# Optimization experiments

Hardware: AMD Instinct MI355X
Metric: run time of the kernel (lower is better)

The kernel has to match this reference:

```python
import jax, jax.numpy as jnp
import numpy as np

HIDDEN = 256
HEADS = 8
HEAD_DIM = HIDDEN // HEADS


def setup_inputs() -> dict:
    key = jax.random.key(0)
    ks = jax.random.split(key, 8)
    B, N, L, C = 8, 512, 24, HIDDEN
    s = 1.0 / np.sqrt(C)
    return {
        "spatial_nodes": jax.random.normal(ks[0], (B, N, C), jnp.float32),
        "temporal_nodes": jax.random.normal(ks[1], (B, N, L, C), jnp.float32),
        "Wq": jax.random.normal(ks[2], (C, C), jnp.float32) * s,
        "bq": jnp.zeros((C,), jnp.float32),
        "Wkv": jax.random.normal(ks[3], (C, 2 * C), jnp.float32) * s,
        "bkv": jnp.zeros((2 * C,), jnp.float32),
        "Wo": jax.random.normal(ks[4], (C, C), jnp.float32) * s,
        "bo": jnp.zeros((C,), jnp.float32),
    }


def reference(spatial_nodes, temporal_nodes, Wq, bq, Wkv, bkv, Wo, bo):
    B, N, C = spatial_nodes.shape
    L = temporal_nodes.shape[2]
    H, D = HEADS, HEAD_DIM
    q = spatial_nodes @ Wq + bq                      # [B,N,C]
    kv = temporal_nodes @ Wkv + bkv                  # [B,N,L,2C]
    k, v = jnp.split(kv, 2, axis=-1)                 # each [B,N,L,C]
    q = q.reshape(B, N, H, D)
    k = k.reshape(B, N, L, H, D)
    v = v.reshape(B, N, L, H, D)
    scores = jnp.einsum('bnhd,bnlhd->bnhl', q, k) / jnp.sqrt(jnp.float32(D))
    attn = jax.nn.softmax(scores, axis=-1)           # dropout is identity in eval
    out = jnp.einsum('bnhl,bnlhd->bnhd', attn, v).reshape(B, N, C)
    return out @ Wo + bo
```

## Files before the change

### kernel.cpp

```cpp
#include <hip/hip_runtime.h>
#include <hip/hip_bf16.h>


#define L_ 24
#define C_ 256
#define H_ 8
#define D_ 32
#define NTOK 4096
#define SCALE 0.17677669529663687f

typedef __attribute__((ext_vector_type(8))) short short8;
typedef __attribute__((ext_vector_type(4))) float f32x4;

#define QK_OFF   ((size_t)0)
#define TBAR_OFF ((size_t)16777216)
#define MT_OFF   ((size_t)33554432)
#define W2T_OFF  ((size_t)34603008)
#define BQK_OFF  ((size_t)35651584)
#define BO2_OFF  ((size_t)35659776)
#define WS_NEED  ((size_t)35660800)

__global__ __launch_bounds__(256)
void k_pre(const float* __restrict__ Wq, const float* __restrict__ bq,
           const float* __restrict__ Wkv, const float* __restrict__ bkv,
           const float* __restrict__ Wo, const float* __restrict__ bo,
           char* __restrict__ ws)
{
    __hip_bfloat16* mt  = (__hip_bfloat16*)(ws + MT_OFF);
    __hip_bfloat16* w2t = (__hip_bfloat16*)(ws + W2T_OFF);
    float* bqk = (float*)(ws + BQK_OFF);
    float* bo2 = (float*)(ws + BO2_OFF);
    const int b = blockIdx.x, tid = threadIdx.x;
    __shared__ float sW[32][33];
    if (b < 128) {
        const bool isV = b >= 64;
        const int bb = isV ? b - 64 : b;
        const int h = bb >> 3, c0 = (bb & 7) * 32;
        {
            const int ci = tid >> 3, dq = (tid & 7) * 4;
            const float4 v = *(const float4*)(Wkv + (size_t)(c0 + ci) * 512 + (isV ? 256 : 0) + h * 32 + dq);
            sW[ci][dq + 0] = v.x; sW[ci][dq + 1] = v.y; sW[ci][dq + 2] = v.z; sW[ci][dq + 3] = v.w;
        }
        __syncthreads();
        const int e = tid;
        float wreg[32];
        if (!isV) {
#pragma unroll
            for (int dq = 0; dq < 32; dq += 4) {
                const float4 v = *(const float4*)(Wq + (size_t)e * 256 + h * 32 + dq);
                wreg[dq] = v.x; wreg[dq + 1] = v.y; wreg[dq + 2] = v.z; wreg[dq + 3] = v.w;
            }
            for (int ci = 0; ci < 32; ++ci) {
                float a = 0.f;
#pragma unroll
                for (int d = 0; d < 32; ++d) a = fmaf(wreg[d], sW[ci][d], a);
                mt[(size_t)(h * 256 + c0 + ci) * 256 + e] = __float2bfloat16(a * SCALE);
            }
        } else {
#pragma unroll
            for (int d = 0; d < 32; ++d) wreg[d] = Wo[(size_t)(h * 32 + d) * 256 + e];
            __hip_bfloat16 accs[32];
            for (int ci = 0; ci < 32; ++ci) {
                float a = 0.f;
#pragma unroll
                for (int d = 0; d < 32; ++d) a = fmaf(wreg[d], sW[ci][d], a);
                accs[ci] = __float2bfloat16(a);
            }
#pragma unroll
            for (int g = 0; g < 4; ++g)
                *(uint4*)&w2t[(size_t)e * 2048 + h * 256 + c0 + g * 8] = *(const uint4*)&accs[g * 8];
        }
    } else if (b == 128) {
        for (int o = 0; o < 8; ++o) {
            const int hc = o * 256 + tid;
            const int h = hc >> 8, c = hc & 255;
            float a = 0.f;
            for (int d = 0; d < 32; ++d)
                a = fmaf(bq[h * 32 + d], Wkv[(size_t)c * 512 + h * 32 + d], a);
            bqk[hc] = a * SCALE;
        }
    } else {
        const int e = tid;
        float a = bo[e];
        for (int hd = 0; hd < 256; ++hd)
            a = fmaf(bkv[256 + hd], Wo[(size_t)hd * 256 + e], a);
        bo2[e] = a;
    }
}

__global__ __launch_bounds__(256)
void k_qk(const float* __restrict__ S, char* __restrict__ ws)
{
    const __hip_bfloat16* mt = (const __hip_bfloat16*)(ws + MT_OFF);
    const float* bqk = (const float*)(ws + BQK_OFF);
    __hip_bfloat16* qk = (__hip_bfloat16*)(ws + QK_OFF);
    __shared__ __hip_bfloat16 sA[64][40];
    __shared__ __hip_bfloat16 sB[64][40];
    const int tid = threadIdx.x;
    const int bm = blockIdx.x & 63, bn = blockIdx.x >> 6;
    const int m0 = bm * 64, n0 = bn * 64;
    const int w = tid >> 6, L = tid & 63;
    const int wr = (w >> 1) * 32, wc = (w & 1) * 32;
    const int fr = L & 15, fk = (L >> 4) * 8;
    const int sr = tid >> 2, sc = (tid & 3) * 8;
    f32x4 acc[2][2] = {};
    for (int k0 = 0; k0 < 256; k0 += 32) {
        {
            const float* p = S + (size_t)(m0 + sr) * 256 + k0 + sc;
            const float4 v0 = *(const float4*)p, v1 = *(const float4*)(p + 4);
            union { __hip_bfloat16 h[8]; uint4 u; } pk;
            pk.h[0] = __float2bfloat16(v0.x); pk.h[1] = __float2bfloat16(v0.y);
            pk.h[2] = __float2bfloat16(v0.z); pk.h[3] = __float2bfloat16(v0.w);
            pk.h[4] = __float2bfloat16(v1.x); pk.h[5] = __float2bfloat16(v1.y);
            pk.h[6] = __float2bfloat16(v1.z); pk.h[7] = __float2bfloat16(v1.w);
            *(uint4*)&sA[sr][sc] = pk.u;
            *(uint4*)&sB[sr][sc] = *(const uint4*)(mt + (size_t)(n0 + sr) * 256 + k0 + sc);
        }
        __syncthreads();
        short8 af0 = *(const short8*)&sA[wr +  0 + fr][fk];
        short8 af1 = *(const short8*)&sA[wr + 16 + fr][fk];
        short8 bf0 = *(const short8*)&sB[wc +  0 + fr][fk];
        short8 bf1 = *(const short8*)&sB[wc + 16 + fr][fk];
        acc[0][0] = __builtin_amdgcn_mfma_f32_16x16x32_bf16(af0, bf0, acc[0][0], 0, 0, 0);
        acc[0][1] = __builtin_amdgcn_mfma_f32_16x16x32_bf16(af0, bf1, acc[0][1], 0, 0, 0);
        acc[1][0] = __builtin_amdgcn_mfma_f32_16x16x32_bf16(af1, bf0, acc[1][0], 0, 0, 0);
        acc[1][1] = __builtin_amdgcn_mfma_f32_16x16x32_bf16(af1, bf1, acc[1][1], 0, 0, 0);
        __syncthreads();
    }
#pragma unroll
    for (int i = 0; i < 2; ++i)
#pragma unroll
    for (int j = 0; j < 2; ++j) {
        const int col = n0 + wc + j * 16 + fr;
        const float bb = bqk[col];
#pragma unroll
        for (int r = 0; r < 4; ++r) {
            const int row = m0 + wr + i * 16 + (L >> 4) * 4 + r;
            qk[(size_t)row * 2048 + col] = __float2bfloat16(acc[i][j][r] + bb);
        }
    }
}

__global__ __launch_bounds__(256)
void k_attn(const float* __restrict__ T, char* __restrict__ ws)
{
    const __hip_bfloat16* qk = (const __hip_bfloat16*)(ws + QK_OFF);
    __hip_bfloat16* tbar = (__hip_bfloat16*)(ws + TBAR_OFF);
    __shared__ float            sT[24][260];
    __shared__ __hip_bfloat16   sTb[32][264];
    __shared__ __hip_bfloat16   sqk[16][264];
    __shared__ float            sAt[8][33];
    const int tid = threadIdx.x;
    const int t = blockIdx.x;
    {
        const float4* Tv = (const float4*)(T + (size_t)t * 6144);
#pragma unroll
        for (int k = 0; k < 6; ++k) {
            const int f = tid + k * 256;
            const float4 v = Tv[f];
            const int l = f >> 6, c = (f & 63) * 4;
            *(float4*)&sT[l][c] = v;
            __hip_bfloat16 b4[4] = { __float2bfloat16(v.x), __float2bfloat16(v.y),
                                     __float2bfloat16(v.z), __float2bfloat16(v.w) };
            *(uint2*)&sTb[l][c] = *(const uint2*)b4;
        }
    }
    {
        const int h = tid >> 5, c = (tid & 31) * 8;
        *(uint4*)&sqk[h][c] = *(const uint4*)(qk + (size_t)t * 2048 + tid * 8);
    }
    {
        const uint4 z = {0u, 0u, 0u, 0u};
        char* zq = (char*)&sqk[8][0];
        char* zt = (char*)&sTb[24][0];
        *(uint4*)(zq + tid * 16) = z;
        *(uint4*)(zt + tid * 16) = z;
        if (tid < 8) {
            *(uint4*)(zq + 4096 + tid * 16) = z;
            *(uint4*)(zt + 4096 + tid * 16) = z;
        }
    }
    __syncthreads();
    if (tid < 64) {
        const int fr = tid & 15, fk = (tid >> 4) * 8;
        f32x4 acc[2] = {};
#pragma unroll
        for (int ks = 0; ks < 8; ++ks) {
            const short8 a  = *(const short8*)&sqk[fr][ks * 32 + fk];
            const short8 b0 = *(const short8*)&sTb[fr][ks * 32 + fk];
            const short8 b1 = *(const short8*)&sTb[16 + fr][ks * 32 + fk];
            acc[0] = __builtin_amdgcn_mfma_f32_16x16x32_bf16(a, b0, acc[0], 0, 0, 0);
            acc[1] = __builtin_amdgcn_mfma_f32_16x16x32_bf16(a, b1, acc[1], 0, 0, 0);
        }
        if (tid < 32) {
            const int hb = (tid >> 4) * 4, l0 = tid & 15;
#pragma unroll
            for (int r = 0; r < 4; ++r) {
                sAt[hb + r][l0] = acc[0][r];
                if (l0 < 8) sAt[hb + r][16 + l0] = acc[1][r];
            }
        }
    }
    __syncthreads();
    if (tid < 8) {
        float mx = -1e30f;
#pragma unroll
        for (int l = 0; l < 24; ++l) mx = fmaxf(mx, sAt[tid][l]);
        float e[24]; float sum = 0.f;
#pragma unroll
        for (int l = 0; l < 24; ++l) { e[l] = __expf(sAt[tid][l] - mx); sum += e[l]; }
        const float inv = 1.0f / sum;
#pragma unroll
        for (int l = 0; l < 24; ++l) sAt[tid][l] = e[l] * inv;
    }
    __syncthreads();
    {
        const int h = tid >> 5, c0 = (tid & 31) * 8;
        float acc[8] = {};
        for (int l = 0; l < 24; ++l) {
            const float a = sAt[h][l];
            const float4 u = *(const float4*)&sT[l][c0];
            const float4 v = *(const float4*)&sT[l][c0 + 4];
            acc[0] = fmaf(a, u.x, acc[0]); acc[1] = fmaf(a, u.y, acc[1]);
            acc[2] = fmaf(a, u.z, acc[2]); acc[3] = fmaf(a, u.w, acc[3]);
            acc[4] = fmaf(a, v.x, acc[4]); acc[5] = fmaf(a, v.y, acc[5]);
            acc[6] = fmaf(a, v.z, acc[6]); acc[7] = fmaf(a, v.w, acc[7]);
        }
        union { __hip_bfloat16 h8[8]; uint4 u; } pk;
#pragma unroll
        for (int j = 0; j < 8; ++j) pk.h8[j] = __float2bfloat16(acc[j]);
        *(uint4*)&tbar[(size_t)t * 2048 + tid * 8] = pk.u;
    }
}

__global__ __launch_bounds__(256)
void k_out(const char* __restrict__ ws, float* __restrict__ Out)
{
    const __hip_bfloat16* tbar = (const __hip_bfloat16*)(ws + TBAR_OFF);
    const __hip_bfloat16* w2t  = (const __hip_bfloat16*)(ws + W2T_OFF);
    const float* bo2 = (const float*)(ws + BO2_OFF);
    __shared__ __hip_bfloat16 sA[64][72];
    __shared__ __hip_bfloat16 sB[32][72];
    const int tid = threadIdx.x;
    const int bm = blockIdx.x & 63, bn = blockIdx.x >> 6;
    const int m0 = bm * 64, n0 = bn * 32;
    const int w = tid >> 6, L = tid & 63;
    const int fr = L & 15, fkb = (L >> 4) * 8;
    const int ar = tid >> 2, ac = (tid & 3) * 16;
    const int br = tid >> 3, bc = (tid & 7) * 8;
    f32x4 acc[2] = {};
    for (int k0 = 0; k0 < 2048; k0 += 64) {
        {
            const uint4* pa = (const uint4*)(tbar + (size_t)(m0 + ar) * 2048 + k0 + ac);
            *(uint4*)&sA[ar][ac]     = pa[0];
            *(uint4*)&sA[ar][ac + 8] = pa[1];
            *(uint4*)&sB[br][bc] = *(const uint4*)(w2t + (size_t)(n0 + br) * 2048 + k0 + bc);
        }
        __syncthreads();
#pragma unroll
        for (int half = 0; half < 2; ++half) {
            const int kb = half * 32 + fkb;
            const short8 af = *(const short8*)&sA[w * 16 + fr][kb];
            const short8 b0 = *(const short8*)&sB[ 0 + fr][kb];
            const short8 b1 = *(const short8*)&sB[16 + fr][kb];
            acc[0] = __builtin_amdgcn_mfma_f32_16x16x32_bf16(af, b0, acc[0], 0, 0, 0);
            acc[1] = __builtin_amdgcn_mfma_f32_16x16x32_bf16(af, b1, acc[1], 0, 0, 0);
        }
        __syncthreads();
    }
#pragma unroll
    for (int j = 0; j < 2; ++j) {
        const int col = n0 + j * 16 + fr;
        const float bb = bo2[col];
#pragma unroll
        for (int r = 0; r < 4; ++r) {
            const int row = m0 + w * 16 + (L >> 4) * 4 + r;
            Out[(size_t)row * 256 + col] = acc[j][r] + bb;
        }
    }
}

#define NT    16
#define NTHR  512
#define NBLK  256
#define TSTR  (C_ + 4)
#define QKSTR (C_ + 8)
#define QSTR  (D_ + 4)
#define WKROW 268

__global__ __launch_bounds__(NTHR)
void t2s_attn_fused(const float* __restrict__ S, const float* __restrict__ T,
                    const float* __restrict__ Wq, const float* __restrict__ bq,
                    const float* __restrict__ Wkv, const float* __restrict__ bkv,
                    const float* __restrict__ Wo, const float* __restrict__ bo,
                    float* __restrict__ Out)
{
    __shared__ float            sQ[NT][H_][QSTR];
    __shared__ float            sWk[16 * WKROW];
    __shared__ float            sT[2][L_][TSTR];
    __shared__ __hip_bfloat16   sQKT[NT][H_][QKSTR];
    __shared__ float            sSc[H_][L_ + 8];
    const int tid = threadIdx.x;
    const int g0  = blockIdx.x * NT;
    float4 tp0, tp1, tp2;
    {
        const float* tb = T + (size_t)g0 * (L_ * C_);
        tp0 = *(const float4*)(tb + 0 * 2048 + tid * 4);
        tp1 = *(const float4*)(tb + 1 * 2048 + tid * 4);
        tp2 = *(const float4*)(tb + 2 * 2048 + tid * 4);
    }
    {
        const int col = tid & 255;
        const int t0  = (tid >> 8) * 8;
        float acc[8];
        const float bqv = bq[col];
#pragma unroll
        for (int j = 0; j < 8; ++j) acc[j] = bqv;
        const float* sp = S + (size_t)(g0 + t0) * C_;
        for (int c = 0; c < C_; ++c) {
            const float w = Wq[c * C_ + col];
#pragma unroll
            for (int j = 0; j < 8; ++j)
                acc[j] = fmaf(sp[j * C_ + c], w, acc[j]);
        }
#pragma unroll
        for (int j = 0; j < 8; ++j)
            sQ[t0 + j][col >> 5][col & 31] = acc[j];
    }
    {
        const int e = tid * 4;
        *(float4*)&sT[0][(e >> 8) +  0][e & 255] = tp0;
        *(float4*)&sT[0][(e >> 8) +  8][e & 255] = tp1;
        *(float4*)&sT[0][(e >> 8) + 16][e & 255] = tp2;
    }
    __syncthreads();
    {
        const int cq = tid & 3;
        const int h  = (tid >> 2) & 7;
        const int t  = tid >> 5;
        for (int ct = 0; ct < 16; ++ct) {
            {
                const int hd  = tid & 255, ci2 = tid >> 8;
                const float* wsrc = Wkv + (size_t)(ct * 16) * 512;
#pragma unroll
                for (int j = 0; j < 8; ++j) {
                    const int ci = ci2 + j * 2;
                    sWk[ci * WKROW + (hd >> 5) * 33 + (hd & 31)] = wsrc[(size_t)ci * 512 + hd];
                }
            }
            __syncthreads();
            float a0 = 0.f, a1 = 0.f, a2 = 0.f, a3 = 0.f;
            const float* qrow = &sQ[t][h][0];
            const float* wb   = &sWk[(cq * 4) * WKROW + h * 33];
#pragma unroll
            for (int d = 0; d < D_; ++d) {
                const float qv = qrow[d];
                a0 = fmaf(qv, wb[0 * WKROW + d], a0);
                a1 = fmaf(qv, wb[1 * WKROW + d], a1);
                a2 = fmaf(qv, wb[2 * WKROW + d], a2);
                a3 = fmaf(qv, wb[3 * WKROW + d], a3);
            }
            const int c0 = ct * 16 + cq * 4;
            sQKT[t][h][c0 + 0] = __float2bfloat16(a0);
            sQKT[t][h][c0 + 1] = __float2bfloat16(a1);
            sQKT[t][h][c0 + 2] = __float2bfloat16(a2);
            sQKT[t][h][c0 + 3] = __float2bfloat16(a3);
            __syncthreads();
        }
    }
    const int lane = tid & 63, wav = tid >> 6;
    for (int t = 0; t < NT; ++t) {
        const int cur = t & 1;
        const bool pf = (t + 1 < NT);
        if (pf) {
            const float* tb = T + (size_t)(g0 + t + 1) * (L_ * C_);
            tp0 = *(const float4*)(tb + 0 * 2048 + tid * 4);
            tp1 = *(const float4*)(tb + 1 * 2048 + tid * 4);
            tp2 = *(const float4*)(tb + 2 * 2048 + tid * 4);
        }
        if (tid < 192) {
            const int h = tid / 24, l = tid - h * 24;
            const float* trow = &sT[cur][l][0];
            const unsigned short* qkr = (const unsigned short*)&sQKT[t][h][0];
            float a0 = 0.f, a1 = 0.f, a2 = 0.f, a3 = 0.f;
            for (int c = 0; c < C_; c += 4) {
                const float4 tv = *(const float4*)(trow + c);
                const uint2  qu = *(const uint2*)(qkr + c);
                a0 = fmaf(tv.x, __uint_as_float(qu.x << 16),          a0);
                a1 = fmaf(tv.y, __uint_as_float(qu.x & 0xffff0000u), a1);
                a2 = fmaf(tv.z, __uint_as_float(qu.y << 16),          a2);
                a3 = fmaf(tv.w, __uint_as_float(qu.y & 0xffff0000u), a3);
            }
            sSc[h][l] = (a0 + a1 + a2 + a3) * 0.17677669529663687f;
        }
        __syncthreads();
        if (tid < 8) {
            float mx = -1e30f;
#pragma unroll
            for (int l = 0; l < L_; ++l) mx = fmaxf(mx, sSc[tid][l]);
            float e[L_]; float sum = 0.f;
#pragma unroll
            for (int l = 0; l < L_; ++l) { e[l] = __expf(sSc[tid][l] - mx); sum += e[l]; }
            const float inv = 1.0f / sum;
#pragma unroll
            for (int l = 0; l < L_; ++l) sSc[tid][l] = e[l] * inv;
        }
        __syncthreads();
        {
            const int h = wav, c0 = lane * 4;
            float ax = 0.f, ay = 0.f, az = 0.f, aw = 0.f;
            const float* at = &sSc[h][0];
#pragma unroll
            for (int l = 0; l < L_; ++l) {
                const float  a  = at[l];
                const float4 tv = *(const float4*)&sT[cur][l][c0];
                ax = fmaf(a, tv.x, ax); ay = fmaf(a, tv.y, ay);
                az = fmaf(a, tv.z, az); aw = fmaf(a, tv.w, aw);
            }
            sQKT[t][h][c0 + 0] = __float2bfloat16(ax);
            sQKT[t][h][c0 + 1] = __float2bfloat16(ay);
            sQKT[t][h][c0 + 2] = __float2bfloat16(az);
            sQKT[t][h][c0 + 3] = __float2bfloat16(aw);
        }
        if (pf) {
            const int e = tid * 4;
            *(float4*)&sT[cur ^ 1][(e >> 8) +  0][e & 255] = tp0;
            *(float4*)&sT[cur ^ 1][(e >> 8) +  8][e & 255] = tp1;
            *(float4*)&sT[cur ^ 1][(e >> 8) + 16][e & 255] = tp2;
        }
        __syncthreads();
    }
    {
        const int hd = tid & 255;
        const int h  = hd >> 5;
        const int t0 = (tid >> 8) * 8;
        float acc[8];
        const float bv = bkv[C_ + hd];
#pragma unroll
        for (int j = 0; j < 8; ++j) acc[j] = bv;
        const float* wv = Wkv + C_ + hd;
        for (int c = 0; c < C_; c += 2) {
            const float w0 = wv[(size_t)c * 512];
            const float w1 = wv[(size_t)(c + 1) * 512];
#pragma unroll
            for (int j = 0; j < 8; ++j) {
                const unsigned int u = *(const unsigned int*)&sQKT[t0 + j][h][c];
                acc[j] = fmaf(__uint_as_float(u << 16),          w0, acc[j]);
                acc[j] = fmaf(__uint_as_float(u & 0xffff0000u), w1, acc[j]);
            }
        }
#pragma unroll
        for (int j = 0; j < 8; ++j)
            sQ[t0 + j][h][hd & 31] = acc[j];
    }
    __syncthreads();
    {
        const int col = tid & 255;
        const int t0  = (tid >> 8) * 8;
        float acc[8];
        const float bov = bo[col];
#pragma unroll
        for (int j = 0; j < 8; ++j) acc[j] = bov;
        for (int hd = 0; hd < C_; ++hd) {
            const float w  = Wo[hd * C_ + col];
            const int  hh = hd >> 5, dd = hd & 31;
#pragma unroll
            for (int j = 0; j < 8; ++j)
                acc[j] = fmaf(sQ[t0 + j][hh][dd], w, acc[j]);
        }
#pragma unroll
        for (int j = 0; j < 8; ++j)
            Out[(size_t)(g0 + t0 + j) * C_ + col] = acc[j];
    }
}

extern "C" void kernel_launch(void* const* d_in, const int* in_sizes, int n_in,
                              void* d_out, int out_size, void* d_ws, size_t ws_size,
                              hipStream_t stream) {
    const float* S   = (const float*)d_in[0];
    const float* T   = (const float*)d_in[1];
    const float* Wq  = (const float*)d_in[2];
    const float* bq  = (const float*)d_in[3];
    const float* Wkv = (const float*)d_in[4];
    const float* bkv = (const float*)d_in[5];
    const float* Wo  = (const float*)d_in[6];
    const float* bo  = (const float*)d_in[7];
    float* Out = (float*)d_out;
    if (ws_size >= WS_NEED) {
        char* ws = (char*)d_ws;
        hipLaunchKernelGGL(k_pre,  dim3(130),  dim3(256), 0, stream, Wq, bq, Wkv, bkv, Wo, bo, ws);
        hipLaunchKernelGGL(k_qk,   dim3(2048), dim3(256), 0, stream, S, ws);
        hipLaunchKernelGGL(k_attn, dim3(4096), dim3(256), 0, stream, T, ws);
        hipLaunchKernelGGL(k_out,  dim3(512),  dim3(256), 0, stream, ws, Out);
    } else {
        hipLaunchKernelGGL(t2s_attn_fused, dim3(NBLK), dim3(NTHR), 0, stream,
                           S, T, Wq, bq, Wkv, bkv, Wo, bo, Out);
    }
}
```

Baseline: 80.18 us.

## Deepen K tiles in GEMMs, vectorize bias precompute, drop fp32 T copy in attention

The QK and output GEMM kernels now stage twice as much of K per iteration (64 and 128), halving the loop trips and barrier pairs. The attention kernel drops the fp32 shared copy of the temporal tile and reads V from the bf16 copy, expanding it to fp32 in registers. This cuts shared memory use and stores, but makes the AV product use bf16-rounded values. The bias-fold precompute is also reworked to use float4 row loads.

```diff
diff --git a/kernel.cpp b/kernel.cpp
--- a/kernel.cpp
+++ b/kernel.cpp
@@ -71,13 +71,20 @@
                 *(uint4*)&w2t[(size_t)e * 2048 + h * 256 + c0 + g * 8] = *(const uint4*)&accs[g * 8];
         }
     } else if (b == 128) {
-        for (int o = 0; o < 8; ++o) {
-            const int hc = o * 256 + tid;
-            const int h = hc >> 8, c = hc & 255;
+        const int c = tid;
+        const float* row = Wkv + (size_t)c * 512;
+#pragma unroll
+        for (int h = 0; h < 8; ++h) {
             float a = 0.f;
-            for (int d = 0; d < 32; ++d)
-                a = fmaf(bq[h * 32 + d], Wkv[(size_t)c * 512 + h * 32 + d], a);
-            bqk[hc] = a * SCALE;
+#pragma unroll
+            for (int dq = 0; dq < 32; dq += 4) {
+                const float4 v = *(const float4*)(row + h * 32 + dq);
+                a = fmaf(bq[h * 32 + dq + 0], v.x, a);
+                a = fmaf(bq[h * 32 + dq + 1], v.y, a);
+                a = fmaf(bq[h * 32 + dq + 2], v.z, a);
+                a = fmaf(bq[h * 32 + dq + 3], v.w, a);
+            }
+            bqk[h * 256 + c] = a * SCALE;
         }
     } else {
         const int e = tid;
@@ -94,37 +101,47 @@
     const __hip_bfloat16* mt = (const __hip_bfloat16*)(ws + MT_OFF);
     const float* bqk = (const float*)(ws + BQK_OFF);
     __hip_bfloat16* qk = (__hip_bfloat16*)(ws + QK_OFF);
-    __shared__ __hip_bfloat16 sA[64][40];
-    __shared__ __hip_bfloat16 sB[64][40];
+    __shared__ __hip_bfloat16 sA[64][72];
+    __shared__ __hip_bfloat16 sB[64][72];
     const int tid = threadIdx.x;
     const int bm = blockIdx.x & 63, bn = blockIdx.x >> 6;
     const int m0 = bm * 64, n0 = bn * 64;
     const int w = tid >> 6, L = tid & 63;
     const int wr = (w >> 1) * 32, wc = (w & 1) * 32;
     const int fr = L & 15, fk = (L >> 4) * 8;
-    const int sr = tid >> 2, sc = (tid & 3) * 8;
+    const int sr = tid >> 2, sc = (tid & 3) * 16;
     f32x4 acc[2][2] = {};
-    for (int k0 = 0; k0 < 256; k0 += 32) {
+    for (int k0 = 0; k0 < 256; k0 += 64) {
         {
             const float* p = S + (size_t)(m0 + sr) * 256 + k0 + sc;
-            const float4 v0 = *(const float4*)p, v1 = *(const float4*)(p + 4);
-            union { __hip_bfloat16 h[8]; uint4 u; } pk;
-            pk.h[0] = __float2bfloat16(v0.x); pk.h[1] = __float2bfloat16(v0.y);
-            pk.h[2] = __float2bfloat16(v0.z); pk.h[3] = __float2bfloat16(v0.w);
-            pk.h[4] = __float2bfloat16(v1.x); pk.h[5] = __float2bfloat16(v1.y);
-            pk.h[6] = __float2bfloat16(v1.z); pk.h[7] = __float2bfloat16(v1.w);
-            *(uint4*)&sA[sr][sc] = pk.u;
-            *(uint4*)&sB[sr][sc] = *(const uint4*)(mt + (size_t)(n0 + sr) * 256 + k0 + sc);
-        }
-        __syncthreads();
-        short8 af0 = *(const short8*)&sA[wr +  0 + fr][fk];
-        short8 af1 = *(const short8*)&sA[wr + 16 + fr][fk];
-        short8 bf0 = *(const short8*)&sB[wc +  0 + fr][fk];
-        short8 bf1 = *(const short8*)&sB[wc + 16 + fr][fk];
-        acc[0][0] = __builtin_amdgcn_mfma_f32_16x16x32_bf16(af0, bf0, acc[0][0], 0, 0, 0);
-        acc[0][1] = __builtin_amdgcn_mfma_f32_16x16x32_bf16(af0, bf1, acc[0][1], 0, 0, 0);
-        acc[1][0] = __builtin_amdgcn_mfma_f32_16x16x32_bf16(af1, bf0, acc[1][0], 0, 0, 0);
-        acc[1][1] = __builtin_amdgcn_mfma_f32_16x16x32_bf16(af1, bf1, acc[1][1], 0, 0, 0);
+            union { __hip_bfloat16 h[16]; uint4 u[2]; } pk;
+#pragma unroll
+            for (int q = 0; q < 4; ++q) {
+                const float4 v = *(const float4*)(p + q * 4);
+                pk.h[q * 4 + 0] = __float2bfloat16(v.x);
+                pk.h[q * 4 + 1] = __float2bfloat16(v.y);
+                pk.h[q * 4 + 2] = __float2bfloat16(v.z);
+                pk.h[q * 4 + 3] = __float2bfloat16(v.w);
+            }
+            *(uint4*)&sA[sr][sc]     = pk.u[0];
+            *(uint4*)&sA[sr][sc + 8] = pk.u[1];
+            const uint4* pb = (const uint4*)(mt + (size_t)(n0 + sr) * 256 + k0 + sc);
+            *(uint4*)&sB[sr][sc]     = pb[0];
+            *(uint4*)&sB[sr][sc + 8] = pb[1];
+        }
+        __syncthreads();
+#pragma unroll
+        for (int kh = 0; kh < 2; ++kh) {
+            const int fk2 = kh * 32 + fk;
+            const short8 af0 = *(const short8*)&sA[wr +  0 + fr][fk2];
+            const short8 af1 = *(const short8*)&sA[wr + 16 + fr][fk2];
+            const short8 bf0 = *(const short8*)&sB[wc +  0 + fr][fk2];
+            const short8 bf1 = *(const short8*)&sB[wc + 16 + fr][fk2];
+            acc[0][0] = __builtin_amdgcn_mfma_f32_16x16x32_bf16(af0, bf0, acc[0][0], 0, 0, 0);
+            acc[0][1] = __builtin_amdgcn_mfma_f32_16x16x32_bf16(af0, bf1, acc[0][1], 0, 0, 0);
+            acc[1][0] = __builtin_amdgcn_mfma_f32_16x16x32_bf16(af1, bf0, acc[1][0], 0, 0, 0);
+            acc[1][1] = __builtin_amdgcn_mfma_f32_16x16x32_bf16(af1, bf1, acc[1][1], 0, 0, 0);
+        }
         __syncthreads();
     }
 #pragma unroll
@@ -146,7 +163,6 @@
 {
     const __hip_bfloat16* qk = (const __hip_bfloat16*)(ws + QK_OFF);
     __hip_bfloat16* tbar = (__hip_bfloat16*)(ws + TBAR_OFF);
-    __shared__ float            sT[24][260];
     __shared__ __hip_bfloat16   sTb[32][264];
     __shared__ __hip_bfloat16   sqk[16][264];
     __shared__ float            sAt[8][33];
@@ -159,7 +175,6 @@
             const int f = tid + k * 256;
             const float4 v = Tv[f];
             const int l = f >> 6, c = (f & 63) * 4;
-            *(float4*)&sT[l][c] = v;
             __hip_bfloat16 b4[4] = { __float2bfloat16(v.x), __float2bfloat16(v.y),
                                      __float2bfloat16(v.z), __float2bfloat16(v.w) };
             *(uint2*)&sTb[l][c] = *(const uint2*)b4;
@@ -219,12 +234,13 @@
         float acc[8] = {};
         for (int l = 0; l < 24; ++l) {
             const float a = sAt[h][l];
-            const float4 u = *(const float4*)&sT[l][c0];
-            const float4 v = *(const float4*)&sT[l][c0 + 4];
-            acc[0] = fmaf(a, u.x, acc[0]); acc[1] = fmaf(a, u.y, acc[1]);
-            acc[2] = fmaf(a, u.z, acc[2]); acc[3] = fmaf(a, u.w, acc[3]);
-            acc[4] = fmaf(a, v.x, acc[4]); acc[5] = fmaf(a, v.y, acc[5]);
-            acc[6] = fmaf(a, v.z, acc[6]); acc[7] = fmaf(a, v.w, acc[7]);
+            const uint4 v = *(const uint4*)&sTb[l][c0];
+            const unsigned int* pu = (const unsigned int*)&v;
+#pragma unroll
+            for (int j = 0; j < 4; ++j) {
+                acc[2 * j]     = fmaf(a, __uint_as_float(pu[j] << 16),          acc[2 * j]);
+                acc[2 * j + 1] = fmaf(a, __uint_as_float(pu[j] & 0xffff0000u), acc[2 * j + 1]);
+            }
         }
         union { __hip_bfloat16 h8[8]; uint4 u; } pk;
 #pragma unroll
@@ -239,27 +255,30 @@
     const __hip_bfloat16* tbar = (const __hip_bfloat16*)(ws + TBAR_OFF);
     const __hip_bfloat16* w2t  = (const __hip_bfloat16*)(ws + W2T_OFF);
     const float* bo2 = (const float*)(ws + BO2_OFF);
-    __shared__ __hip_bfloat16 sA[64][72];
-    __shared__ __hip_bfloat16 sB[32][72];
+    __shared__ __hip_bfloat16 sA[64][136];
+    __shared__ __hip_bfloat16 sB[32][136];
     const int tid = threadIdx.x;
     const int bm = blockIdx.x & 63, bn = blockIdx.x >> 6;
     const int m0 = bm * 64, n0 = bn * 32;
     const int w = tid >> 6, L = tid & 63;
     const int fr = L & 15, fkb = (L >> 4) * 8;
-    const int ar = tid >> 2, ac = (tid & 3) * 16;
-    const int br = tid >> 3, bc = (tid & 7) * 8;
+    const int ar = tid >> 2, ac = (tid & 3) * 32;
+    const int br = tid >> 3, bc = (tid & 7) * 16;
     f32x4 acc[2] = {};
-    for (int k0 = 0; k0 < 2048; k0 += 64) {
+    for (int k0 = 0; k0 < 2048; k0 += 128) {
         {
             const uint4* pa = (const uint4*)(tbar + (size_t)(m0 + ar) * 2048 + k0 + ac);
-            *(uint4*)&sA[ar][ac]     = pa[0];
-            *(uint4*)&sA[ar][ac + 8] = pa[1];
-            *(uint4*)&sB[br][bc] = *(const uint4*)(w2t + (size_t)(n0 + br) * 2048 + k0 + bc);
-        }
-        __syncthreads();
-#pragma unroll
-        for (int half = 0; half < 2; ++half) {
-            const int kb = half * 32 + fkb;
+#pragma unroll
+            for (int q = 0; q < 4; ++q)
+                *(uint4*)&sA[ar][ac + q * 8] = pa[q];
+            const uint4* pb = (const uint4*)(w2t + (size_t)(n0 + br) * 2048 + k0 + bc);
+            *(uint4*)&sB[br][bc]     = pb[0];
+            *(uint4*)&sB[br][bc + 8] = pb[1];
+        }
+        __syncthreads();
+#pragma unroll
+        for (int sub = 0; sub < 4; ++sub) {
+            const int kb = sub * 32 + fkb;
             const short8 af = *(const short8*)&sA[w * 16 + fr][kb];
             const short8 b0 = *(const short8*)&sB[ 0 + fr][kb];
             const short8 b1 = *(const short8*)&sB[16 + fr][kb];
```

Result: faster. 71.44 us (-10.9%).
